# Kernel tuning notes

Measured on AMD Instinct MI355X. Metric: run time of the kernel, lower is better.

## Reference

```python
import jax, jax.numpy as jnp
import numpy as np

B, F, N = 32, 10, 512   # batch_num, win_size (all_feature), node_num
E = 8192                # edges per graph
INTER = 256             # GAT inter_dim
HEADS = 2
NEG_SLOPE = 0.2
BN_EPS = 1e-5


def setup_inputs() -> dict:
    key = jax.random.key(0)
    ks = jax.random.split(key, 16)
    data = jax.random.normal(ks[0], (B, F, N), dtype=jnp.float32)
    # loop-free random edges: src != dst (matches PyG remove_self_loops + add_self_loops)
    dst = jax.random.randint(ks[1], (E,), 0, N)
    off = jax.random.randint(ks[2], (E,), 1, N)
    src = (dst + off) % N
    org_edge_index = jnp.stack([src, dst]).astype(jnp.int64)
    g = 0.05
    return {
        "data": data,
        "org_edge_index": org_edge_index,
        "W1": jax.random.normal(ks[3], (F, HEADS * INTER), dtype=jnp.float32) * g,
        "as1": jax.random.normal(ks[4], (HEADS, INTER), dtype=jnp.float32) * g,
        "ad1": jax.random.normal(ks[5], (HEADS, INTER), dtype=jnp.float32) * g,
        "b1": jnp.zeros((HEADS * INTER,), dtype=jnp.float32),
        "W2": jax.random.normal(ks[6], (HEADS * INTER, HEADS * INTER), dtype=jnp.float32) * g,
        "as2": jax.random.normal(ks[7], (HEADS, INTER), dtype=jnp.float32) * g,
        "ad2": jax.random.normal(ks[8], (HEADS, INTER), dtype=jnp.float32) * g,
        "b2": jnp.zeros((HEADS * INTER,), dtype=jnp.float32),
        "Wfc": jax.random.normal(ks[9], (HEADS * INTER, 1), dtype=jnp.float32) * g,
        "bfc": jnp.zeros((1,), dtype=jnp.float32),
        "gamma": jnp.ones((1,), dtype=jnp.float32),
        "beta": jnp.zeros((1,), dtype=jnp.float32),
    }


def _gat_conv(x, src, dst, W, a_src, a_dst, b):
    # PyG GATConv (v1), concat=True, negative_slope=0.2
    n = x.shape[0]
    H, C = a_src.shape
    h = (x @ W).reshape(n, H, C)                       # [n, H, C]
    al_s = jnp.einsum('nhc,hc->nh', h, a_src)          # [n, H]
    al_d = jnp.einsum('nhc,hc->nh', h, a_dst)
    e = jax.nn.leaky_relu(al_s[src] + al_d[dst], NEG_SLOPE)  # [Etot, H]
    emax = jax.ops.segment_max(e, dst, num_segments=n)       # segment softmax over dst
    ex = jnp.exp(e - emax[dst])
    denom = jax.ops.segment_sum(ex, dst, num_segments=n)
    alpha = ex / (denom[dst] + 1e-16)                  # [Etot, H]
    msg = h[src] * alpha[:, :, None]                   # [Etot, H, C]
    out = jax.ops.segment_sum(msg, dst, num_segments=n)
    return out.reshape(n, H * C) + b


def reference(data, org_edge_index, W1, as1, ad1, b1, W2, as2, ad2, b2,
              Wfc, bfc, gamma, beta):
    b_num, feat, n_num = data.shape
    x = data.reshape(-1, feat)                         # faithful to x.view(-1, all_feature)
    total = b_num * n_num
    # batched edge index: repeat with per-batch node offsets
    offs = jnp.arange(b_num, dtype=org_edge_index.dtype) * n_num
    be = (org_edge_index[:, None, :] + offs[None, :, None]).reshape(2, -1)
    loops = jnp.arange(total, dtype=org_edge_index.dtype)  # add_self_loops
    src = jnp.concatenate([be[0], loops])
    dst = jnp.concatenate([be[1], loops])
    x1 = _gat_conv(x, src, dst, W1, as1, ad1, b1)      # dropout = identity (eval)
    x2 = _gat_conv(x1, src, dst, W2, as2, ad2, b2)
    y = x2 @ Wfc + bfc                                 # [total, 1]
    # BatchNorm1d(1), eval mode: running_mean=0, running_var=1
    y = y * (gamma / jnp.sqrt(1.0 + BN_EPS)) + beta
    y = jax.nn.relu(y)
    return y.reshape(-1, 1, n_num)                     # [B, 1, N]
```

## Files before the change

### kernel.cpp

```cpp
#include <hip/hip_runtime.h>
#include <math.h>

#define B_  32
#define F_  10
#define N_  512
#define E_  8192
#define T_  16384
#define EC_ 8704
#define HC_ 512
#define C_  256

typedef __attribute__((ext_vector_type(8))) short bf16x8;
typedef __attribute__((ext_vector_type(4))) float f32x4;

__device__ __forceinline__ unsigned short f2bf(float f) {
    unsigned int u = __float_as_uint(f);
    u = (u + 0x7fffu + ((u >> 16) & 1u)) >> 16;
    return (unsigned short)u;
}
__device__ __forceinline__ float bf2f(unsigned short b) {
    return __uint_as_float(((unsigned int)b) << 16);
}
__device__ __forceinline__ float dot4(f32x4 a, f32x4 b) {
    f32x4 m = a * b;
    return m[0] + m[1] + m[2] + m[3];
}
__device__ __forceinline__ unsigned int pack2(unsigned short a, unsigned short b) {
    return (unsigned int)a | ((unsigned int)b << 16);
}
__device__ __forceinline__ void bf2x2(unsigned int u, float& f0, float& f1) {
    f0 = __uint_as_float(u << 16);
    f1 = __uint_as_float(u & 0xffff0000u);
}
__device__ __forceinline__ void async_cp16(const void* g, void* l) {
    __builtin_amdgcn_global_load_lds(
        (const __attribute__((address_space(1))) unsigned int*)g,
        (__attribute__((address_space(3))) unsigned int*)l, 16, 0, 0);
}

__device__ __forceinline__ int node_map(int bid, int wid) {
    int x = bid & 7;
    int rest = bid >> 3;
    int batch = x * 4 + (rest >> 7);
    int within = rest & 127;
    return batch * 512 + within * 4 + wid;
}

__global__ __launch_bounds__(1024) void prep_kernel(
    const int* __restrict__ eidx, const float* __restrict__ W2,
    int* __restrict__ off0, int* __restrict__ csr0,
    unsigned short* __restrict__ Bhi, unsigned short* __restrict__ Blo) {
    if (blockIdx.x < 256) {
        __shared__ float t[32][33];
        int bx = blockIdx.x & 15, by = blockIdx.x >> 4;
        int kb = bx * 32, nb = by * 32;
        int tx = threadIdx.x & 31, r = threadIdx.x >> 5;
        t[r][tx] = W2[(size_t)(kb + r) * HC_ + nb + tx];
        __syncthreads();
        float v = t[tx][r];
        unsigned short h = f2bf(v);
        Bhi[(size_t)(nb + r) * HC_ + kb + tx] = h;
        Blo[(size_t)(nb + r) * HC_ + kb + tx] = f2bf(v - bf2f(h));
    } else {
        __shared__ int cnt[512];
        __shared__ int scn[512];
        int tid = threadIdx.x;
        if (tid < 512) cnt[tid] = 0;
        __syncthreads();
        const int* edst = eidx + E_;
        for (int j = tid; j < EC_; j += 1024) {
            int d = (j < E_) ? edst[j] : (j - E_);
            atomicAdd(&cnt[d], 1);
        }
        __syncthreads();
        if (tid < 512) scn[tid] = cnt[tid];
        __syncthreads();
        for (int dd = 1; dd < 512; dd <<= 1) {
            int add = (tid < 512 && tid >= dd) ? scn[tid - dd] : 0;
            __syncthreads();
            if (tid < 512) scn[tid] += add;
            __syncthreads();
        }
        if (tid < 512) {
            int excl = scn[tid] - cnt[tid];
            off0[tid] = excl;
            cnt[tid] = excl;
        }
        if (tid == 0) off0[512] = EC_;
        __syncthreads();
        for (int j = tid; j < EC_; j += 1024) {
            int s, d;
            if (j < E_) { s = eidx[j]; d = edst[j]; }
            else { s = d = j - E_; }
            int pos = atomicAdd(&cnt[d], 1);
            csr0[pos] = s;
        }
    }
}

__global__ __launch_bounds__(256) void gemm1_kernel(
    const float* __restrict__ X, const float* __restrict__ W1,
    const float* __restrict__ a_s, const float* __restrict__ a_d,
    unsigned short* __restrict__ Hs, float* __restrict__ als,
    float* __restrict__ ald, float* __restrict__ als2z,
    float* __restrict__ ald2z) {
    int tid = threadIdx.x, lane = tid & 63, wid = tid >> 6;
    int node = node_map(blockIdx.x, wid);
    int col = lane * 8;
    float x[F_];
    const float* xp = X + (size_t)node * F_;
#pragma unroll
    for (int k = 0; k < F_; ++k) x[k] = xp[k];
    f32x4 h0 = {0.f, 0.f, 0.f, 0.f}, h1 = h0;
#pragma unroll
    for (int k = 0; k < F_; ++k) {
        f32x4 w0 = *(const f32x4*)&W1[k * HC_ + col];
        f32x4 w1 = *(const f32x4*)&W1[k * HC_ + col + 4];
        h0 += x[k] * w0;
        h1 += x[k] * w1;
    }
    uint4 uh;
    uh.x = pack2(f2bf(h0[0]), f2bf(h0[1]));
    uh.y = pack2(f2bf(h0[2]), f2bf(h0[3]));
    uh.z = pack2(f2bf(h1[0]), f2bf(h1[1]));
    uh.w = pack2(f2bf(h1[2]), f2bf(h1[3]));
    *(uint4*)&Hs[(size_t)node * HC_ + col] = uh;
    float ps = dot4(h0, *(const f32x4*)&a_s[col]) + dot4(h1, *(const f32x4*)&a_s[col + 4]);
    float pd = dot4(h0, *(const f32x4*)&a_d[col]) + dot4(h1, *(const f32x4*)&a_d[col + 4]);
#pragma unroll
    for (int m = 1; m <= 16; m <<= 1) {
        ps += __shfl_xor(ps, m);
        pd += __shfl_xor(pd, m);
    }
    if (lane == 0)  { als[node * 2 + 0] = ps; ald[node * 2 + 0] = pd; }
    if (lane == 32) { als[node * 2 + 1] = ps; ald[node * 2 + 1] = pd; }
    if (lane == 16) {
        *(float2*)&als2z[node * 2] = make_float2(0.f, 0.f);
        *(float2*)&ald2z[node * 2] = make_float2(0.f, 0.f);
    }
}

template <int MODE>
__global__ __launch_bounds__(256) void agg_kernel(
    const unsigned short* __restrict__ Hin, const float* __restrict__ als,
    const float* __restrict__ ald, const int* __restrict__ off0,
    const int* __restrict__ csr0, const float* __restrict__ bias,
    unsigned short* __restrict__ Ahi,
    const float* __restrict__ Wfc, const float* __restrict__ bfc,
    const float* __restrict__ gamma, const float* __restrict__ beta,
    float* __restrict__ out) {
    int tid = threadIdx.x, lane = tid & 63, wid = tid >> 6;
    int dst = node_map(blockIdx.x, wid);
    int bbase = dst & ~511;
    int dl = dst & 511;
    int beg = off0[dl], end = off0[dl + 1], deg = end - beg;
    float ad0 = ald[2 * dst], ad1 = ald[2 * dst + 1];
    int col = lane * 8;
    float A[8] = {0.f, 0.f, 0.f, 0.f, 0.f, 0.f, 0.f, 0.f};

    if (deg <= 64) {
        float e0 = -1e30f, e1 = -1e30f;
        int sl = 0;
        if (lane < deg) {
            sl = csr0[beg + lane] + bbase;
            float a0 = als[2 * sl], a1 = als[2 * sl + 1];
            e0 = a0 + ad0; e0 = e0 > 0.f ? e0 : 0.2f * e0;
            e1 = a1 + ad1; e1 = e1 > 0.f ? e1 : 0.2f * e1;
        }
        float m0 = e0, m1 = e1;
#pragma unroll
        for (int m = 1; m < 64; m <<= 1) {
            m0 = fmaxf(m0, __shfl_xor(m0, m));
            m1 = fmaxf(m1, __shfl_xor(m1, m));
        }
        float x0 = (lane < deg) ? expf(e0 - m0) : 0.f;
        float x1 = (lane < deg) ? expf(e1 - m1) : 0.f;
        float d0 = x0, d1 = x1;
#pragma unroll
        for (int m = 1; m < 64; m <<= 1) {
            d0 += __shfl_xor(d0, m);
            d1 += __shfl_xor(d1, m);
        }
        float w0l = x0 / (d0 + 1e-16f);
        float w1l = x1 / (d1 + 1e-16f);
        for (int e = 0; e < deg; ++e) {
            int s = __shfl(sl, e);
            float wa = __shfl(w0l, e);
            float wb = __shfl(w1l, e);
            float w = (lane < 32) ? wa : wb;
            uint4 hv = *(const uint4*)(Hin + (size_t)s * HC_ + col);
            float f0, f1;
            bf2x2(hv.x, f0, f1); A[0] = fmaf(w, f0, A[0]); A[1] = fmaf(w, f1, A[1]);
            bf2x2(hv.y, f0, f1); A[2] = fmaf(w, f0, A[2]); A[3] = fmaf(w, f1, A[3]);
            bf2x2(hv.z, f0, f1); A[4] = fmaf(w, f0, A[4]); A[5] = fmaf(w, f1, A[5]);
            bf2x2(hv.w, f0, f1); A[6] = fmaf(w, f0, A[6]); A[7] = fmaf(w, f1, A[7]);
        }
    } else {
        float m0 = -1e30f, m1 = -1e30f;
        for (int k = beg + lane; k < end; k += 64) {
            int s = csr0[k] + bbase;
            float e0 = als[2 * s] + ad0; e0 = e0 > 0.f ? e0 : 0.2f * e0;
            float e1 = als[2 * s + 1] + ad1; e1 = e1 > 0.f ? e1 : 0.2f * e1;
            m0 = fmaxf(m0, e0);
            m1 = fmaxf(m1, e1);
        }
#pragma unroll
        for (int m = 1; m < 64; m <<= 1) {
            m0 = fmaxf(m0, __shfl_xor(m0, m));
            m1 = fmaxf(m1, __shfl_xor(m1, m));
        }
        float d0 = 0.f, d1 = 0.f;
        for (int k = beg + lane; k < end; k += 64) {
            int s = csr0[k] + bbase;
            float e0 = als[2 * s] + ad0; e0 = e0 > 0.f ? e0 : 0.2f * e0;
            float e1 = als[2 * s + 1] + ad1; e1 = e1 > 0.f ? e1 : 0.2f * e1;
            d0 += expf(e0 - m0);
            d1 += expf(e1 - m1);
        }
#pragma unroll
        for (int m = 1; m < 64; m <<= 1) {
            d0 += __shfl_xor(d0, m);
            d1 += __shfl_xor(d1, m);
        }
        float inv0 = 1.f / (d0 + 1e-16f);
        float inv1 = 1.f / (d1 + 1e-16f);
        for (int k = beg; k < end; ++k) {
            int s = csr0[k] + bbase;
            float e0 = als[2 * s] + ad0; e0 = e0 > 0.f ? e0 : 0.2f * e0;
            float e1 = als[2 * s + 1] + ad1; e1 = e1 > 0.f ? e1 : 0.2f * e1;
            float w0 = expf(e0 - m0) * inv0;
            float w1 = expf(e1 - m1) * inv1;
            float w = (lane < 32) ? w0 : w1;
            uint4 hv = *(const uint4*)(Hin + (size_t)s * HC_ + col);
            float f0, f1;
            bf2x2(hv.x, f0, f1); A[0] = fmaf(w, f0, A[0]); A[1] = fmaf(w, f1, A[1]);
            bf2x2(hv.y, f0, f1); A[2] = fmaf(w, f0, A[2]); A[3] = fmaf(w, f1, A[3]);
            bf2x2(hv.z, f0, f1); A[4] = fmaf(w, f0, A[4]); A[5] = fmaf(w, f1, A[5]);
            bf2x2(hv.w, f0, f1); A[6] = fmaf(w, f0, A[6]); A[7] = fmaf(w, f1, A[7]);
        }
    }

#pragma unroll
    for (int j = 0; j < 8; ++j) A[j] += bias[col + j];

    if (MODE == 0) {
        uint4 uh;
        uh.x = pack2(f2bf(A[0]), f2bf(A[1]));
        uh.y = pack2(f2bf(A[2]), f2bf(A[3]));
        uh.z = pack2(f2bf(A[4]), f2bf(A[5]));
        uh.w = pack2(f2bf(A[6]), f2bf(A[7]));
        *(uint4*)&Ahi[(size_t)dst * HC_ + col] = uh;
    } else {
        float y = 0.f;
#pragma unroll
        for (int j = 0; j < 8; ++j) y = fmaf(A[j], Wfc[col + j], y);
#pragma unroll
        for (int m = 1; m < 64; m <<= 1) y += __shfl_xor(y, m);
        if (lane == 0) {
            y += bfc[0];
            y = y * (gamma[0] * rsqrtf(1.f + 1e-5f)) + beta[0];
            out[dst] = y > 0.f ? y : 0.f;
        }
    }
}

__global__ __launch_bounds__(512, 1) void gemm2_kernel(
    const unsigned short* __restrict__ Ahi,
    const unsigned short* __restrict__ Bhi, const unsigned short* __restrict__ Blo,
    unsigned short* __restrict__ H2,
    const float* __restrict__ as2, const float* __restrict__ ad2,
    float* __restrict__ als2, float* __restrict__ ald2) {
    __shared__ __align__(16) char smem[135168];
    const int tid = threadIdx.x, lane = tid & 63, wid = tid >> 6;
    const int wr = wid >> 1, wc = wid & 1;
    const int g = (blockIdx.x & 7) * 32 + (blockIdx.x >> 3);
    const int row0 = (g >> 2) * 256, col0 = (g & 3) * 128;
    const int lr = lane & 15, lk = lane >> 4;
    const int x7 = lr & 7;

    f32x4 acc[4][4] = {};

    const char* gsrc[8];
    int loff[8];
#pragma unroll
    for (int l = 0; l < 8; ++l) {
        int i = tid + l * 512;
        if (i < 2048) {
            int r = i >> 3, c = i & 7;
            gsrc[l] = (const char*)(Ahi + (size_t)(row0 + r) * HC_ + ((c ^ (r & 7)) << 3));
            loff[l] = i << 4;
        } else if (i < 3072) {
            int j = i - 2048, r = j >> 3, c = j & 7;
            gsrc[l] = (const char*)(Bhi + (size_t)(col0 + r) * HC_ + ((c ^ (r & 7)) << 3));
            loff[l] = 32768 + (j << 4);
        } else {
            int j = i - 3072, r = j >> 3, c = j & 7;
            gsrc[l] = (const char*)(Blo + (size_t)(col0 + r) * HC_ + ((c ^ (r & 7)) << 3));
            loff[l] = 49152 + (j << 4);
        }
    }
    char* lds0 = smem;

#pragma unroll
    for (int l = 0; l < 8; ++l) async_cp16(gsrc[l], lds0 + loff[l]);
    asm volatile("s_waitcnt vmcnt(0)" ::: "memory");
    __builtin_amdgcn_s_barrier();

    int cur = 0;
    for (int kt = 0; kt < 8; ++kt) {
        if (kt < 7) {
            char* dst = lds0 + ((cur ^ 1) << 16);
#pragma unroll
            for (int l = 0; l < 8; ++l)
                async_cp16(gsrc[l] + (size_t)(kt + 1) * 128, dst + loff[l]);
        }
        const char* base = lds0 + (cur << 16);
#pragma unroll
        for (int kk = 0; kk < 2; ++kk) {
            bf16x8 a[4], bh[4], bl[4];
            int cx = ((kk * 4 + lk) ^ x7) << 4;
#pragma unroll
            for (int m = 0; m < 4; ++m) {
                int ra = wr * 64 + m * 16 + lr;
                int rb = wc * 64 + m * 16 + lr;
                a[m]  = *(const bf16x8*)(base + ra * 128 + cx);
                bh[m] = *(const bf16x8*)(base + 32768 + rb * 128 + cx);
                bl[m] = *(const bf16x8*)(base + 49152 + rb * 128 + cx);
            }
#pragma unroll
            for (int m = 0; m < 4; ++m)
#pragma unroll
                for (int n = 0; n < 4; ++n) {
                    acc[m][n] = __builtin_amdgcn_mfma_f32_16x16x32_bf16(a[m], bh[n], acc[m][n], 0, 0, 0);
                    acc[m][n] = __builtin_amdgcn_mfma_f32_16x16x32_bf16(a[m], bl[n], acc[m][n], 0, 0, 0);
                }
        }
        asm volatile("s_waitcnt vmcnt(0)" ::: "memory");
        __builtin_amdgcn_s_barrier();
        cur ^= 1;
    }

    float* tb = (float*)smem;
#pragma unroll
    for (int m = 0; m < 4; ++m)
#pragma unroll
        for (int i = 0; i < 4; ++i) {
            int row = wr * 64 + m * 16 + lk * 4 + i;
#pragma unroll
            for (int n = 0; n < 4; ++n)
                tb[row * 132 + wc * 64 + n * 16 + lr] = acc[m][n][i];
        }
    __syncthreads();
    const int head = col0 >> 8;
    const float* a_s2 = as2 + head * C_ + (col0 & 255);
    const float* a_d2 = ad2 + head * C_ + (col0 & 255);
#pragma unroll
    for (int p = 0; p < 8; ++p) {
        int q = tid + p * 512;
        int row = q >> 4, cs = (q & 15) * 8;
        const float* v = &tb[row * 132 + cs];
        uint4 uh;
        uh.x = pack2(f2bf(v[0]), f2bf(v[1]));
        uh.y = pack2(f2bf(v[2]), f2bf(v[3]));
        uh.z = pack2(f2bf(v[4]), f2bf(v[5]));
        uh.w = pack2(f2bf(v[6]), f2bf(v[7]));
        *(uint4*)&H2[(size_t)(row0 + row) * HC_ + col0 + cs] = uh;
        float ps = 0.f, pd = 0.f;
#pragma unroll
        for (int j = 0; j < 8; ++j) {
            ps = fmaf(v[j], a_s2[cs + j], ps);
            pd = fmaf(v[j], a_d2[cs + j], pd);
        }
#pragma unroll
        for (int m = 1; m < 16; m <<= 1) {
            ps += __shfl_xor(ps, m);
            pd += __shfl_xor(pd, m);
        }
        if ((tid & 15) == 0) {
            atomicAdd(&als2[(row0 + row) * 2 + head], ps);
            atomicAdd(&ald2[(row0 + row) * 2 + head], pd);
        }
    }
}

extern "C" void kernel_launch(void* const* d_in, const int* in_sizes, int n_in,
                              void* d_out, int out_size, void* d_ws, size_t ws_size,
                              hipStream_t stream) {
    const float* data  = (const float*)d_in[0];
    const int*   eidx  = (const int*)d_in[1];
    const float* W1    = (const float*)d_in[2];
    const float* as1   = (const float*)d_in[3];
    const float* ad1   = (const float*)d_in[4];
    const float* b1    = (const float*)d_in[5];
    const float* W2    = (const float*)d_in[6];
    const float* as2   = (const float*)d_in[7];
    const float* ad2   = (const float*)d_in[8];
    const float* b2    = (const float*)d_in[9];
    const float* Wfc   = (const float*)d_in[10];
    const float* bfc   = (const float*)d_in[11];
    const float* gamma = (const float*)d_in[12];
    const float* beta  = (const float*)d_in[13];
    float* out = (float*)d_out;

    char* base = (char*)d_ws;
    size_t o = 0;
    auto take = [&](size_t bytes) {
        char* p = base + o;
        o = (o + bytes + 255) & ~(size_t)255;
        return p;
    };
    int*   off0 = (int*)take((size_t)(N_ + 1) * 4);
    int*   csr0 = (int*)take((size_t)EC_ * 4);
    float* als1 = (float*)take((size_t)T_ * 2 * 4);
    float* ald1 = (float*)take((size_t)T_ * 2 * 4);
    float* als2 = (float*)take((size_t)T_ * 2 * 4);
    float* ald2 = (float*)take((size_t)T_ * 2 * 4);
    unsigned short* hs1 = (unsigned short*)take((size_t)T_ * HC_ * 2);
    unsigned short* hs2 = (unsigned short*)take((size_t)T_ * HC_ * 2);
    unsigned short* Ahi = (unsigned short*)take((size_t)T_ * HC_ * 2);
    unsigned short* Bhi = (unsigned short*)take((size_t)HC_ * HC_ * 2);
    unsigned short* Blo = (unsigned short*)take((size_t)HC_ * HC_ * 2);

    prep_kernel<<<257, 1024, 0, stream>>>(eidx, W2, off0, csr0, Bhi, Blo);
    gemm1_kernel<<<4096, 256, 0, stream>>>(data, W1, as1, ad1, hs1, als1, ald1,
                                           als2, ald2);
    agg_kernel<0><<<4096, 256, 0, stream>>>(hs1, als1, ald1, off0, csr0, b1,
                                            Ahi, nullptr, nullptr, nullptr,
                                            nullptr, nullptr);
    gemm2_kernel<<<256, 512, 0, stream>>>(Ahi, Bhi, Blo, hs2, as2, ad2, als2, ald2);
    agg_kernel<1><<<4096, 256, 0, stream>>>(hs2, als2, ald2, off0, csr0, b2,
                                            nullptr, Wfc, bfc, gamma,
                                            beta, out);
}
```

Before: 99.88 us.

## Fold prep work into gemm1 launch and software-pipeline neighbor loads in aggregation

The separate prep kernel (W2 transpose/bf16 split and CSR build) is merged into gemm1 as 257 extra blocks of 256 threads, removing one kernel launch and letting prep overlap with the gemm1 work. The aggregation loop over neighbors now prefetches the next neighbor's feature row and weight before accumulating the current one, hiding gather latency. The CSR build now runs in a single 256-thread block, which lengthens that serial path, and gemm1 gains a shared-memory footprint that may reduce occupancy.

Result: slower. 108.1 us (+8.2%).

```diff
diff --git a/kernel.cpp b/kernel.cpp
--- a/kernel.cpp
+++ b/kernel.cpp
@@ -46,65 +46,75 @@
     return batch * 512 + within * 4 + wid;
 }
 
-__global__ __launch_bounds__(1024) void prep_kernel(
-    const int* __restrict__ eidx, const float* __restrict__ W2,
-    int* __restrict__ off0, int* __restrict__ csr0,
-    unsigned short* __restrict__ Bhi, unsigned short* __restrict__ Blo) {
-    if (blockIdx.x < 256) {
-        __shared__ float t[32][33];
-        int bx = blockIdx.x & 15, by = blockIdx.x >> 4;
-        int kb = bx * 32, nb = by * 32;
-        int tx = threadIdx.x & 31, r = threadIdx.x >> 5;
-        t[r][tx] = W2[(size_t)(kb + r) * HC_ + nb + tx];
-        __syncthreads();
-        float v = t[tx][r];
-        unsigned short h = f2bf(v);
-        Bhi[(size_t)(nb + r) * HC_ + kb + tx] = h;
-        Blo[(size_t)(nb + r) * HC_ + kb + tx] = f2bf(v - bf2f(h));
-    } else {
-        __shared__ int cnt[512];
-        __shared__ int scn[512];
-        int tid = threadIdx.x;
-        if (tid < 512) cnt[tid] = 0;
-        __syncthreads();
-        const int* edst = eidx + E_;
-        for (int j = tid; j < EC_; j += 1024) {
-            int d = (j < E_) ? edst[j] : (j - E_);
-            atomicAdd(&cnt[d], 1);
-        }
-        __syncthreads();
-        if (tid < 512) scn[tid] = cnt[tid];
-        __syncthreads();
-        for (int dd = 1; dd < 512; dd <<= 1) {
-            int add = (tid < 512 && tid >= dd) ? scn[tid - dd] : 0;
-            __syncthreads();
-            if (tid < 512) scn[tid] += add;
-            __syncthreads();
-        }
-        if (tid < 512) {
-            int excl = scn[tid] - cnt[tid];
-            off0[tid] = excl;
-            cnt[tid] = excl;
-        }
-        if (tid == 0) off0[512] = EC_;
-        __syncthreads();
-        for (int j = tid; j < EC_; j += 1024) {
-            int s, d;
-            if (j < E_) { s = eidx[j]; d = edst[j]; }
-            else { s = d = j - E_; }
-            int pos = atomicAdd(&cnt[d], 1);
-            csr0[pos] = s;
-        }
-    }
-}
-
 __global__ __launch_bounds__(256) void gemm1_kernel(
     const float* __restrict__ X, const float* __restrict__ W1,
     const float* __restrict__ a_s, const float* __restrict__ a_d,
     unsigned short* __restrict__ Hs, float* __restrict__ als,
     float* __restrict__ ald, float* __restrict__ als2z,
-    float* __restrict__ ald2z) {
-    int tid = threadIdx.x, lane = tid & 63, wid = tid >> 6;
+    float* __restrict__ ald2z,
+    const int* __restrict__ eidx, const float* __restrict__ W2,
+    int* __restrict__ off0, int* __restrict__ csr0,
+    unsigned short* __restrict__ Bhi, unsigned short* __restrict__ Blo) {
+    __shared__ int shmem[1200];
+    int tid = threadIdx.x;
+
+    if (blockIdx.x >= 4096) {
+        int pb = blockIdx.x - 4096;
+        if (pb < 256) {
+            float* t = (float*)shmem;
+            int bx = pb & 15, by = pb >> 4;
+            int kb = bx * 32, nb = by * 32;
+            int tx = tid & 31, ty = tid >> 5;
+#pragma unroll
+            for (int r = ty; r < 32; r += 8)
+                t[r * 33 + tx] = W2[(size_t)(kb + r) * HC_ + nb + tx];
+            __syncthreads();
+#pragma unroll
+            for (int r = ty; r < 32; r += 8) {
+                float v = t[tx * 33 + r];
+                unsigned short h = f2bf(v);
+                Bhi[(size_t)(nb + r) * HC_ + kb + tx] = h;
+                Blo[(size_t)(nb + r) * HC_ + kb + tx] = f2bf(v - bf2f(h));
+            }
+        } else {
+            int* cnt = shmem;
+            int* scn = shmem + 512;
+            for (int i = tid; i < 512; i += 256) cnt[i] = 0;
+            __syncthreads();
+            const int* edst = eidx + E_;
+            for (int j = tid; j < EC_; j += 256) {
+                int d = (j < E_) ? edst[j] : (j - E_);
+                atomicAdd(&cnt[d], 1);
+            }
+            __syncthreads();
+            int c0 = cnt[2 * tid], c1 = cnt[2 * tid + 1];
+            scn[tid] = c0 + c1;
+            __syncthreads();
+            for (int d = 1; d < 256; d <<= 1) {
+                int add = (tid >= d) ? scn[tid - d] : 0;
+                __syncthreads();
+                scn[tid] += add;
+                __syncthreads();
+            }
+            int e0 = scn[tid] - (c0 + c1);
+            off0[2 * tid] = e0;
+            off0[2 * tid + 1] = e0 + c0;
+            cnt[2 * tid] = e0;
+            cnt[2 * tid + 1] = e0 + c0;
+            if (tid == 255) off0[512] = EC_;
+            __syncthreads();
+            for (int j = tid; j < EC_; j += 256) {
+                int s, d;
+                if (j < E_) { s = eidx[j]; d = edst[j]; }
+                else { s = d = j - E_; }
+                int pos = atomicAdd(&cnt[d], 1);
+                csr0[pos] = s;
+            }
+        }
+        return;
+    }
+
+    int lane = tid & 63, wid = tid >> 6;
     int node = node_map(blockIdx.x, wid);
     int col = lane * 8;
     float x[F_];
@@ -183,17 +193,24 @@
         }
         float w0l = x0 / (d0 + 1e-16f);
         float w1l = x1 / (d1 + 1e-16f);
-        for (int e = 0; e < deg; ++e) {
-            int s = __shfl(sl, e);
-            float wa = __shfl(w0l, e);
-            float wb = __shfl(w1l, e);
+        {
+            int sv = __shfl(sl, 0);
+            float wa = __shfl(w0l, 0), wb = __shfl(w1l, 0);
             float w = (lane < 32) ? wa : wb;
-            uint4 hv = *(const uint4*)(Hin + (size_t)s * HC_ + col);
-            float f0, f1;
-            bf2x2(hv.x, f0, f1); A[0] = fmaf(w, f0, A[0]); A[1] = fmaf(w, f1, A[1]);
-            bf2x2(hv.y, f0, f1); A[2] = fmaf(w, f0, A[2]); A[3] = fmaf(w, f1, A[3]);
-            bf2x2(hv.z, f0, f1); A[4] = fmaf(w, f0, A[4]); A[5] = fmaf(w, f1, A[5]);
-            bf2x2(hv.w, f0, f1); A[6] = fmaf(w, f0, A[6]); A[7] = fmaf(w, f1, A[7]);
+            uint4 hv = *(const uint4*)(Hin + (size_t)sv * HC_ + col);
+            for (int e = 0; e < deg; ++e) {
+                int en = (e + 1 < deg) ? e + 1 : 0;
+                int sn = __shfl(sl, en);
+                float wan = __shfl(w0l, en), wbn = __shfl(w1l, en);
+                float wn = (lane < 32) ? wan : wbn;
+                uint4 hn = *(const uint4*)(Hin + (size_t)sn * HC_ + col);
+                float f0, f1;
+                bf2x2(hv.x, f0, f1); A[0] = fmaf(w, f0, A[0]); A[1] = fmaf(w, f1, A[1]);
+                bf2x2(hv.y, f0, f1); A[2] = fmaf(w, f0, A[2]); A[3] = fmaf(w, f1, A[3]);
+                bf2x2(hv.z, f0, f1); A[4] = fmaf(w, f0, A[4]); A[5] = fmaf(w, f1, A[5]);
+                bf2x2(hv.w, f0, f1); A[6] = fmaf(w, f0, A[6]); A[7] = fmaf(w, f1, A[7]);
+                hv = hn; w = wn;
+            }
         }
     } else {
         float m0 = -1e30f, m1 = -1e30f;
@@ -421,9 +438,9 @@
     unsigned short* Bhi = (unsigned short*)take((size_t)HC_ * HC_ * 2);
     unsigned short* Blo = (unsigned short*)take((size_t)HC_ * HC_ * 2);
 
-    prep_kernel<<<257, 1024, 0, stream>>>(eidx, W2, off0, csr0, Bhi, Blo);
-    gemm1_kernel<<<4096, 256, 0, stream>>>(data, W1, as1, ad1, hs1, als1, ald1,
-                                           als2, ald2);
+    gemm1_kernel<<<4353, 256, 0, stream>>>(data, W1, as1, ad1, hs1, als1, ald1,
+                                           als2, ald2, eidx, W2, off0, csr0,
+                                           Bhi, Blo);
     agg_kernel<0><<<4096, 256, 0, stream>>>(hs1, als1, ald1, off0, csr0, b1,
                                             Ahi, nullptr, nullptr, nullptr,
                                             nullptr, nullptr);
```
